# Performance work log

Measured on AMD Instinct MI355X. Metric: run time of the kernel, lower is better.

## Reference

```python
import jax, jax.numpy as jnp
import numpy as np

N = 50000      # nodes
E = 600000     # edges
F_ATOM = 78
D = 128        # hidden_dim = heads * head_dim
H = 8
C = D // H     # 16
ED = 12        # edge_dim
L = 4          # num_layers
B = 512        # graphs in batch
DFF = 4 * D
SCALE = 1.0 / float(np.sqrt(C))


def setup_inputs() -> dict:
    key = jax.random.key(0)
    ks = iter(jax.random.split(key, 128))
    rn = lambda s, sc=0.05: jax.random.normal(next(ks), s, jnp.float32) * sc
    inp = {
        "x": jax.random.normal(next(ks), (N, F_ATOM), jnp.float32),
        "edge_attr": jax.random.normal(next(ks), (E, ED), jnp.float32),
        "edge_index": jax.random.randint(next(ks), (2, E), 0, N),
        "batch": jnp.sort(jax.random.randint(next(ks), (N,), 0, B)),
        "Wemb": rn((F_ATOM, D)), "bemb": jnp.zeros((D,), jnp.float32),
        "Wout": rn((D, D)), "bout": jnp.zeros((D,), jnp.float32),
    }
    def stk(s, sc=0.05):
        return jnp.stack([rn(s, sc) for _ in range(L)])
    inp.update(
        Wq=stk((D, D)), bq=jnp.zeros((L, D), jnp.float32),
        Wk=stk((D, D)), bk=jnp.zeros((L, D), jnp.float32),
        Wv=stk((D, D)), bv=jnp.zeros((L, D), jnp.float32),
        We=stk((ED, D)), be=jnp.zeros((L, D), jnp.float32),
        Wskip=stk((D, D)), bskip=jnp.zeros((L, D), jnp.float32),
        Wbeta=stk((3 * D,)),
        g1=jnp.ones((L, D), jnp.float32), b1=jnp.zeros((L, D), jnp.float32),
        g2=jnp.ones((L, D), jnp.float32), b2=jnp.zeros((L, D), jnp.float32),
        Wf1=stk((D, DFF)), bf1=jnp.zeros((L, DFF), jnp.float32),
        Wf2=stk((DFF, D)), bf2=jnp.zeros((L, D), jnp.float32),
    )
    return inp


def _ln(x, g, b):
    mu = jnp.mean(x, -1, keepdims=True)
    var = jnp.mean((x - mu) ** 2, -1, keepdims=True)
    return (x - mu) * jax.lax.rsqrt(var + 1e-5) * g + b


def _seg_softmax(alpha, dst):
    # alpha: [E, H]; softmax over edges sharing a destination node
    m = jax.ops.segment_max(alpha, dst, num_segments=N)
    m = jnp.where(jnp.isfinite(m), m, 0.0)
    ex = jnp.exp(alpha - m[dst])
    den = jax.ops.segment_sum(ex, dst, num_segments=N)
    return ex / (den[dst] + 1e-16)


def _forward(x, edge_attr, Wemb, bemb, Wq, bq, Wk, bk, Wv, bv, We, be,
             Wskip, bskip, Wbeta, g1, b1, g2, b2, Wf1, bf1, Wf2, bf2,
             Wout, bout, edge_index, batch):
    src, dst = edge_index[0], edge_index[1]
    h = x @ Wemb + bemb                                    # [N, D]
    for l in range(L):
        q = (h @ Wq[l] + bq[l]).reshape(N, H, C)
        k = (h @ Wk[l] + bk[l]).reshape(N, H, C)
        v = (h @ Wv[l] + bv[l]).reshape(N, H, C)
        e = (edge_attr @ We[l] + be[l]).reshape(E, H, C)
        kj = k[src] + e                                    # [E, H, C]
        alpha = jnp.einsum('ehc,ehc->eh', q[dst], kj) * SCALE
        a = _seg_softmax(alpha, dst)                       # [E, H]
        msg = (v[src] + e) * a[:, :, None]                 # [E, H, C]
        agg = jax.ops.segment_sum(msg, dst, num_segments=N).reshape(N, D)
        xr = h @ Wskip[l] + bskip[l]                       # root/skip transform
        beta = jax.nn.sigmoid(
            jnp.concatenate([agg, xr, agg - xr], -1) @ Wbeta[l])[:, None]
        hc = beta * xr + (1.0 - beta) * agg                # beta gate
        h = _ln(hc + h, g1[l], b1[l])
        ff = jax.nn.relu(h @ Wf1[l] + bf1[l]) @ Wf2[l] + bf2[l]
        h = _ln(ff + h, g2[l], b2[l])
    cnt = jax.ops.segment_sum(jnp.ones((N,), h.dtype), batch, num_segments=B)
    pooled = jax.ops.segment_sum(h, batch, num_segments=B) / jnp.maximum(cnt, 1.0)[:, None]
    return pooled @ Wout + bout                            # [B, D]


def reference(x, edge_attr, edge_index, batch, Wemb, bemb, Wout, bout,
              Wq, bq, Wk, bk, Wv, bv, We, be, Wskip, bskip, Wbeta,
              g1, b1, g2, b2, Wf1, bf1, Wf2, bf2):
    return _forward(x, edge_attr, Wemb, bemb, Wq, bq, Wk, bk, Wv, bv, We, be,
                    Wskip, bskip, Wbeta, g1, b1, g2, b2, Wf1, bf1, Wf2, bf2,
                    Wout, bout, edge_index, batch)
```

## Files before the change

kernel.cpp:

```cpp
#include <hip/hip_runtime.h>
#include <math.h>

#define N_NODES 50000
#define N_EDGES 600000
#define FATOM   78
#define DIM     128
#define HEADS   8
#define EDIM    12
#define LAYERS  4
#define NBATCH  512
#define NDFF    512
#define ASCALE  0.25f

typedef __attribute__((ext_vector_type(8))) short bf16x8;
typedef __attribute__((ext_vector_type(4))) float f32x4;

__device__ __forceinline__ float sum16(float v){
  #pragma unroll
  for (int m=1;m<16;m<<=1) v += __shfl_xor(v, m);
  return v;
}
__device__ __forceinline__ short f2b(float f){
  unsigned int u = __builtin_bit_cast(unsigned int, f);
  u += 0x7fffu + ((u>>16)&1u);
  return (short)(u>>16);
}
__device__ __forceinline__ float b2f_lo(unsigned int u){ return __builtin_bit_cast(float, u<<16); }
__device__ __forceinline__ float b2f_hi(unsigned int u){ return __builtin_bit_cast(float, u & 0xffff0000u); }
__device__ __forceinline__ float b2f_s(short s){
  return __builtin_bit_cast(float, ((unsigned int)(unsigned short)s)<<16);
}
__device__ __forceinline__ void unp8(uint4 u, float* o){
  o[0]=b2f_lo(u.x); o[1]=b2f_hi(u.x); o[2]=b2f_lo(u.y); o[3]=b2f_hi(u.y);
  o[4]=b2f_lo(u.z); o[5]=b2f_hi(u.z); o[6]=b2f_lo(u.w); o[7]=b2f_hi(u.w);
}

__device__ __forceinline__ void gload16(const short* g, short* l){
  __builtin_amdgcn_global_load_lds(
      (const __attribute__((address_space(1))) void*)g,
      (__attribute__((address_space(3))) void*)l, 16, 0, 0);
}

__global__ void count_kernel(const int* __restrict__ ei, int* __restrict__ cnt){
  int e = blockIdx.x*256 + threadIdx.x;
  if (e < N_EDGES) atomicAdd(&cnt[ei[N_EDGES + e]], 1);
}

__global__ __launch_bounds__(1024) void scan1(const int* __restrict__ cnt,
                                              int* __restrict__ row_start, int* __restrict__ bsum){
  __shared__ int lds[1024];
  int gid = blockIdx.x*1024 + threadIdx.x;
  int v = (gid < N_NODES) ? cnt[gid] : 0;
  lds[threadIdx.x] = v; __syncthreads();
  for (int off=1; off<1024; off<<=1){
    int add = (threadIdx.x>=off)?lds[threadIdx.x-off]:0;
    __syncthreads();
    lds[threadIdx.x]+=add;
    __syncthreads();
  }
  if (gid < N_NODES) row_start[gid+1] = lds[threadIdx.x];
  if (threadIdx.x==1023) bsum[blockIdx.x] = lds[1023];
}
__global__ void scan2(int* __restrict__ bsum, int nb){
  int tid = threadIdx.x;
  int v = (tid < nb) ? bsum[tid] : 0;
  #pragma unroll
  for (int off=1; off<64; off<<=1){
    int u = __shfl_up(v, off);
    if (tid >= off) v += u;
  }
  if (tid < nb) bsum[tid] = v;
}
__global__ void scan3(int* __restrict__ row_start, const int* __restrict__ bsum){
  int gid = blockIdx.x*256 + threadIdx.x;
  if (gid == 0) row_start[0] = 0;
  if (gid < N_NODES){
    int blk = gid >> 10;
    if (blk > 0) row_start[gid+1] += bsum[blk-1];
  }
}

__global__ void scatter_kernel(const int* __restrict__ ei, const float* __restrict__ ea,
                               int* __restrict__ cnt2, const int* __restrict__ row_start,
                               int* __restrict__ src_s, short* __restrict__ ea_s){
  int e = blockIdx.x*256 + threadIdx.x;
  if (e < N_EDGES){
    int d = ei[N_EDGES + e];
    int pos = atomicAdd(&cnt2[d], 1);
    int p = row_start[d] + pos;
    src_s[p] = ei[e];
    const float* src = ea + (size_t)e*EDIM;
    unsigned int* dst = (unsigned int*)(ea_s + (size_t)p*EDIM);
    #pragma unroll
    for (int j=0;j<6;j++){
      unsigned int lo = (unsigned int)(unsigned short)f2b(src[2*j]);
      unsigned int hi = (unsigned int)(unsigned short)f2b(src[2*j+1]);
      dst[j] = lo | (hi<<16);
    }
  }
}

__global__ __launch_bounds__(256) void deg_hist(const int* __restrict__ cnt, int* __restrict__ dhist){
  __shared__ int lh[256];
  lh[threadIdx.x] = 0; __syncthreads();
  int n = blockIdx.x*256 + threadIdx.x;
  if (n < N_NODES){
    int d = cnt[n]; if (d > 255) d = 255;
    atomicAdd(&lh[d], 1);
  }
  __syncthreads();
  int c = lh[threadIdx.x];
  if (c) atomicAdd(&dhist[threadIdx.x], c);
}
__global__ __launch_bounds__(256) void deg_scan(const int* __restrict__ dhist, int* __restrict__ dstart){
  __shared__ int l[256];
  int t = threadIdx.x;
  int v = dhist[t];
  l[t] = v; __syncthreads();
  for (int off=1; off<256; off<<=1){
    int add = (t>=off)? l[t-off]:0;
    __syncthreads();
    l[t]+=add;
    __syncthreads();
  }
  dstart[t] = l[t]-v;
}
__global__ __launch_bounds__(256) void deg_place(const int* __restrict__ cnt, int* __restrict__ dcnt,
                                                 const int* __restrict__ dstart, int* __restrict__ perm){
  __shared__ int lh[256];
  __shared__ int lbase[256];
  __shared__ int lrank[256];
  int t = threadIdx.x;
  lh[t] = 0; lrank[t] = 0; __syncthreads();
  int n = blockIdx.x*256 + t;
  int d = -1;
  if (n < N_NODES){
    d = cnt[n]; if (d > 255) d = 255;
    atomicAdd(&lh[d], 1);
  }
  __syncthreads();
  int c = lh[t];
  lbase[t] = c ? atomicAdd(&dcnt[t], c) : 0;
  __syncthreads();
  if (n < N_NODES){
    int r = atomicAdd(&lrank[d], 1);
    perm[dstart[d] + lbase[d] + r] = n;
  }
}

__global__ __launch_bounds__(256) void pack_weights(
  const float* __restrict__ Wq, const float* __restrict__ Wk,
  const float* __restrict__ Wv, const float* __restrict__ Ws,
  const float* __restrict__ bq, const float* __restrict__ bk,
  const float* __restrict__ bv, const float* __restrict__ bs,
  const float* __restrict__ Wf1, const float* __restrict__ Wf2,
  short* __restrict__ wq_t, short* __restrict__ wf1_t, short* __restrict__ wf2_t,
  float* __restrict__ bqkvs)
{
  int l = blockIdx.y;
  int idx = blockIdx.x*256 + threadIdx.x;
  int sec = idx >> 16, r = idx & 65535;
  if (sec == 0){
    int n = r >> 7, k = r & 127;
    const float* W = (n<128)?Wq:(n<256)?Wk:(n<384)?Wv:Ws;
    float v = W[(size_t)l*16384 + k*128 + (n&127)];
    wq_t[(size_t)l*65536 + n*128 + k] = f2b(v);
    if (k == 0){
      const float* bb = (n<128)?bq:(n<256)?bk:(n<384)?bv:bs;
      bqkvs[l*512 + n] = bb[l*128 + (n&127)];
    }
  } else if (sec == 1){
    int n = r >> 7, k = r & 127;
    wf1_t[(size_t)l*65536 + n*128 + k] = f2b(Wf1[(size_t)l*65536 + k*512 + n]);
  } else {
    int n = r >> 9, k = r & 511;
    wf2_t[(size_t)l*65536 + n*512 + k] = f2b(Wf2[(size_t)l*65536 + k*128 + n]);
  }
}

__global__ void pack_emb(const float* __restrict__ Wemb, short* __restrict__ wemb_t){
  int idx = blockIdx.x*256 + threadIdx.x;
  int nn = idx >> 7, k = idx & 127;
  wemb_t[nn*128 + k] = (k < FATOM) ? f2b(Wemb[(size_t)k*DIM + nn]) : (short)0;
}

__global__ void cast_pad_x(const float* __restrict__ x, short* __restrict__ xb){
  int idx = blockIdx.x*256 + threadIdx.x;
  int n = idx >> 6, kp = (idx & 63)*2;
  if (n >= N_NODES) return;
  float v0 = (kp   < FATOM) ? x[(size_t)n*FATOM + kp]   : 0.f;
  float v1 = (kp+1 < FATOM) ? x[(size_t)n*FATOM + kp+1] : 0.f;
  unsigned int lo = (unsigned int)(unsigned short)f2b(v0);
  unsigned int hi = (unsigned int)(unsigned short)f2b(v1);
  *(unsigned int*)(xb + (size_t)n*128 + kp) = lo | (hi<<16);
}

__global__ __launch_bounds__(256) void gemm_k128(
    const short* __restrict__ A,
    const short* __restrict__ Bt,
    const float* __restrict__ bias,
    short* __restrict__ Cb,
    int Nrows, int M, int relu, int nbn)
{
  __shared__ short As[128*128];
  __shared__ short Bs[128*128];
  int tid  = threadIdx.x;
  int lane = tid & 63;
  int wave = tid >> 6;
  int wr = wave >> 1, wc = wave & 1;
  int bm = blockIdx.x * 128;
  int d  = lane & 15;
  int lr = lane >> 4;

  #pragma unroll
  for (int it=0; it<8; ++it){
    int r = wave*32 + it*4 + lr;
    int oct = (d & 8) | ((d & 7) ^ (r & 7));
    int gr = bm + r; if (gr >= Nrows) gr = Nrows-1;
    gload16(A + (size_t)gr*128 + oct*8, As + (wave*32 + it*4)*128);
  }

  for (int t=0; t<nbn; ++t){
    int bn = (blockIdx.y*nbn + t)*128;
    if (t) __syncthreads();
    #pragma unroll
    for (int it=0; it<8; ++it){
      int r = wave*32 + it*4 + lr;
      int oct = (d & 8) | ((d & 7) ^ (r & 7));
      gload16(Bt + (size_t)(bn + r)*128 + oct*8, Bs + (wave*32 + it*4)*128);
    }
    f32x4 zero = {0.f,0.f,0.f,0.f};
    f32x4 acc[4][4];
    #pragma unroll
    for (int m=0;m<4;m++)
      #pragma unroll
      for (int n=0;n<4;n++) acc[m][n] = zero;

    __syncthreads();

    #pragma unroll
    for (int ks=0; ks<4; ++ks){
      int oi = ks*4 + lr;
      bf16x8 af[4], bfv[4];
      #pragma unroll
      for (int m=0;m<4;m++){
        int row = wr*64 + m*16 + d;
        int slot = (oi&8) | ((oi&7) ^ (row&7));
        af[m] = *(const bf16x8*)(As + row*128 + slot*8);
      }
      #pragma unroll
      for (int n=0;n<4;n++){
        int col = wc*64 + n*16 + d;
        int slot = (oi&8) | ((oi&7) ^ (col&7));
        bfv[n] = *(const bf16x8*)(Bs + col*128 + slot*8);
      }
      #pragma unroll
      for (int m=0;m<4;m++)
        #pragma unroll
        for (int n=0;n<4;n++)
          acc[m][n] = __builtin_amdgcn_mfma_f32_16x16x32_bf16(af[m], bfv[n], acc[m][n], 0, 0, 0);
    }

    #pragma unroll
    for (int m=0;m<4;m++){
      #pragma unroll
      for (int n=0;n<4;n++){
        int col = bn + wc*64 + n*16 + d;
        float bval = bias[col];
        #pragma unroll
        for (int j=0;j<4;j++){
          int row = bm + wr*64 + m*16 + lr*4 + j;
          if (row < Nrows){
            float v = acc[m][n][j] + bval;
            if (relu) v = fmaxf(v, 0.f);
            Cb[(size_t)row*M + col] = f2b(v);
          }
        }
      }
    }
  }
}

__global__ __launch_bounds__(256) void gemm_ffn_ln(
    const short* __restrict__ W1t,
    const short* __restrict__ W2t,
    const float* __restrict__ bias1,
    const float* __restrict__ bias2,
    short* __restrict__ hb,
    const float* __restrict__ g, const float* __restrict__ b,
    int Nrows)
{
  __shared__ short As[64*128];
  __shared__ short Bs[128*128];
  __shared__ short F1[64*128];
  __shared__ float red[2][64][2];
  int tid  = threadIdx.x;
  int lane = tid & 63;
  int wave = tid >> 6;
  int wr = wave >> 1, wc = wave & 1;
  int bm = blockIdx.x * 64;
  int d  = lane & 15;
  int lr = lane >> 4;

  #pragma unroll
  for (int it=0; it<4; ++it){
    int rbase = wave*16 + it*4;
    int r = rbase + lr;
    int oct = (d & 8) | ((d & 7) ^ (r & 7));
    int gr = bm + r; if (gr >= Nrows) gr = Nrows-1;
    gload16(hb + (size_t)gr*128 + oct*8, As + rbase*128);
  }

  f32x4 zero = {0.f,0.f,0.f,0.f};
  f32x4 acc2[2][4];
  #pragma unroll
  for (int m=0;m<2;m++)
    #pragma unroll
    for (int n=0;n<4;n++) acc2[m][n] = zero;

  for (int t=0; t<4; ++t){
    #pragma unroll
    for (int it=0; it<8; ++it){
      int rbase = wave*32 + it*4;
      int r = rbase + lr;
      int oct = (d & 8) | ((d & 7) ^ (r & 7));
      gload16(W1t + (size_t)(t*128 + r)*128 + oct*8, Bs + rbase*128);
    }
    __syncthreads();

    f32x4 acc1[2][4];
    #pragma unroll
    for (int m=0;m<2;m++)
      #pragma unroll
      for (int n=0;n<4;n++) acc1[m][n] = zero;
    #pragma unroll
    for (int ks=0; ks<4; ++ks){
      int oi = ks*4 + lr;
      bf16x8 af[2], bfv[4];
      #pragma unroll
      for (int m=0;m<2;m++){
        int row = wr*32 + m*16 + d;
        int slot = (oi&8) | ((oi&7) ^ (row&7));
        af[m] = *(const bf16x8*)(As + row*128 + slot*8);
      }
      #pragma unroll
      for (int n=0;n<4;n++){
        int cn = wc*64 + n*16 + d;
        int slot = (oi&8) | ((oi&7) ^ (cn&7));
        bfv[n] = *(const bf16x8*)(Bs + cn*128 + slot*8);
      }
      #pragma unroll
      for (int m=0;m<2;m++)
        #pragma unroll
        for (int n=0;n<4;n++)
          acc1[m][n] = __builtin_amdgcn_mfma_f32_16x16x32_bf16(af[m], bfv[n], acc1[m][n], 0, 0, 0);
    }
    __syncthreads();

    #pragma unroll
    for (int m=0;m<2;m++){
      #pragma unroll
      for (int n=0;n<4;n++){
        int col = wc*64 + n*16 + d;
        float bv1 = bias1[t*128 + col];
        int oct2 = col >> 3, within = col & 7;
        #pragma unroll
        for (int j=0;j<4;j++){
          int row = wr*32 + m*16 + lr*4 + j;
          float v = fmaxf(acc1[m][n][j] + bv1, 0.f);
          int so = (oct2 & 8) | ((oct2 & 7) ^ (row & 7));
          F1[row*128 + so*8 + within] = f2b(v);
        }
      }
    }
    __syncthreads();

    #pragma unroll
    for (int ks=0; ks<4; ++ks){
      int oi = ks*4 + lr;
      bf16x8 af[2], bfv[4];
      #pragma unroll
      for (int m=0;m<2;m++){
        int row = wr*32 + m*16 + d;
        int slot = (oi&8) | ((oi&7) ^ (row&7));
        af[m] = *(const bf16x8*)(F1 + row*128 + slot*8);
      }
      #pragma unroll
      for (int n=0;n<4;n++){
        int col = wc*64 + n*16 + d;
        bfv[n] = *(const bf16x8*)(W2t + (size_t)col*512 + t*128 + oi*8);
      }
      #pragma unroll
      for (int m=0;m<2;m++)
        #pragma unroll
        for (int n=0;n<4;n++)
          acc2[m][n] = __builtin_amdgcn_mfma_f32_16x16x32_bf16(af[m], bfv[n], acc2[m][n], 0, 0, 0);
    }
  }

  #pragma unroll
  for (int m=0;m<2;m++){
    #pragma unroll
    for (int n=0;n<4;n++){
      int col = wc*64 + n*16 + d;
      float bval = bias2[col];
      #pragma unroll
      for (int j=0;j<4;j++){
        int row = wr*32 + m*16 + lr*4 + j;
        int grow = bm + row; if (grow >= Nrows) grow = Nrows-1;
        acc2[m][n][j] += bval + b2f_s(hb[(size_t)grow*DIM + col]);
      }
    }
  }
  #pragma unroll
  for (int m=0;m<2;m++){
    #pragma unroll
    for (int j=0;j<4;j++){
      float ps = 0.f, pq = 0.f;
      #pragma unroll
      for (int n=0;n<4;n++){ float v = acc2[m][n][j]; ps += v; pq += v*v; }
      #pragma unroll
      for (int msk=1; msk<16; msk<<=1){ ps += __shfl_xor(ps, msk); pq += __shfl_xor(pq, msk); }
      if (d == 0){
        int row = wr*32 + m*16 + lr*4 + j;
        red[wc][row][0] = ps;
        red[wc][row][1] = pq;
      }
    }
  }
  __syncthreads();
  #pragma unroll
  for (int m=0;m<2;m++){
    #pragma unroll
    for (int j=0;j<4;j++){
      int row = wr*32 + m*16 + lr*4 + j;
      float S = red[0][row][0] + red[1][row][0];
      float Q = red[0][row][1] + red[1][row][1];
      float mu  = S*(1.f/128.f);
      float var = fmaxf(Q*(1.f/128.f) - mu*mu, 0.f);
      float rr  = rsqrtf(var + 1e-5f);
      int grow = bm + row;
      if (grow < Nrows){
        #pragma unroll
        for (int n=0;n<4;n++){
          int col = wc*64 + n*16 + d;
          float o = (acc2[m][n][j]-mu)*rr*g[col] + b[col];
          hb[(size_t)grow*DIM + col] = f2b(o);
        }
      }
    }
  }
}

__global__ __launch_bounds__(256) void edge_attn_fused(
  const short* __restrict__ qkvx,
  const short* __restrict__ ea_s, const int* __restrict__ src_s,
  const float* __restrict__ Wel, const float* __restrict__ bel,
  const int* __restrict__ row_start, const int* __restrict__ perm,
  short* __restrict__ hb,
  const float* __restrict__ Wb, const float* __restrict__ g, const float* __restrict__ b)
{
  int wid = (blockIdx.x*256 + threadIdx.x) >> 4;
  if (wid >= N_NODES) return;
  int node = perm[N_NODES - 1 - wid];
  int ln = threadIdx.x & 15;
  int c0 = ln*8;

  const short* qrow = qkvx + (size_t)node*512;
  uint4 qu = *(const uint4*)(qrow + c0);
  float q0=b2f_lo(qu.x), q1=b2f_hi(qu.x), q2=b2f_lo(qu.y), q3=b2f_hi(qu.y);
  float q4=b2f_lo(qu.z), q5=b2f_hi(qu.z), q6=b2f_lo(qu.w), q7=b2f_hi(qu.w);

  float u[12];
  #pragma unroll
  for (int j=0;j<12;j++){
    float4 wA = *(const float4*)(Wel + j*DIM + c0);
    float4 wB = *(const float4*)(Wel + j*DIM + c0 + 4);
    float pp = q0*wA.x+q1*wA.y+q2*wA.z+q3*wA.w
             + q4*wB.x+q5*wB.y+q6*wB.z+q7*wB.w;
    u[j] = pp + __shfl_xor(pp,1);
  }
  float4 beA = *(const float4*)(bel + c0);
  float4 beB = *(const float4*)(bel + c0 + 4);
  float qbe;
  { float pp = q0*beA.x+q1*beA.y+q2*beA.z+q3*beA.w
             + q4*beB.x+q5*beB.y+q6*beB.z+q7*beB.w;
    qbe = pp + __shfl_xor(pp,1); }

  int rs = row_start[node], re = row_start[node+1];
  float den = 0.f;
  float av[8] = {0.f,0.f,0.f,0.f,0.f,0.f,0.f,0.f};
  float aEA[12] = {0.f,0.f,0.f,0.f,0.f,0.f,0.f,0.f,0.f,0.f,0.f,0.f};

  int i = rs;
  for (; i+2 <= re; i += 2){
    int s0 = src_s[i], s1 = src_s[i+1];
    const short* e0p = ea_s + (size_t)i*EDIM;
    uint2 a00 = *(const uint2*)(e0p);
    uint2 a01 = *(const uint2*)(e0p+4);
    uint2 a02 = *(const uint2*)(e0p+8);
    uint2 a10 = *(const uint2*)(e0p+12);
    uint2 a11 = *(const uint2*)(e0p+16);
    uint2 a12 = *(const uint2*)(e0p+20);
    const short* r0p = qkvx + (size_t)s0*512;
    const short* r1p = qkvx + (size_t)s1*512;
    uint4 ku0 = *(const uint4*)(r0p + 128 + c0);
    uint4 vu0 = *(const uint4*)(r0p + 256 + c0);
    uint4 ku1 = *(const uint4*)(r1p + 128 + c0);
    uint4 vu1 = *(const uint4*)(r1p + 256 + c0);

    float ea0[12], ea1[12];
    ea0[0]=b2f_lo(a00.x); ea0[1]=b2f_hi(a00.x); ea0[2]=b2f_lo(a00.y); ea0[3]=b2f_hi(a00.y);
    ea0[4]=b2f_lo(a01.x); ea0[5]=b2f_hi(a01.x); ea0[6]=b2f_lo(a01.y); ea0[7]=b2f_hi(a01.y);
    ea0[8]=b2f_lo(a02.x); ea0[9]=b2f_hi(a02.x); ea0[10]=b2f_lo(a02.y); ea0[11]=b2f_hi(a02.y);
    ea1[0]=b2f_lo(a10.x); ea1[1]=b2f_hi(a10.x); ea1[2]=b2f_lo(a10.y); ea1[3]=b2f_hi(a10.y);
    ea1[4]=b2f_lo(a11.x); ea1[5]=b2f_hi(a11.x); ea1[6]=b2f_lo(a11.y); ea1[7]=b2f_hi(a11.y);
    ea1[8]=b2f_lo(a12.x); ea1[9]=b2f_hi(a12.x); ea1[10]=b2f_lo(a12.y); ea1[11]=b2f_hi(a12.y);

    float pp0 = q0*b2f_lo(ku0.x) + q1*b2f_hi(ku0.x) + q2*b2f_lo(ku0.y) + q3*b2f_hi(ku0.y)
              + q4*b2f_lo(ku0.z) + q5*b2f_hi(ku0.z) + q6*b2f_lo(ku0.w) + q7*b2f_hi(ku0.w);
    float pp1 = q0*b2f_lo(ku1.x) + q1*b2f_hi(ku1.x) + q2*b2f_lo(ku1.y) + q3*b2f_hi(ku1.y)
              + q4*b2f_lo(ku1.z) + q5*b2f_hi(ku1.z) + q6*b2f_lo(ku1.w) + q7*b2f_hi(ku1.w);
    float al0 = pp0 + __shfl_xor(pp0,1) + qbe;
    float al1 = pp1 + __shfl_xor(pp1,1) + qbe;
    #pragma unroll
    for (int j=0;j<12;j++){ al0 += ea0[j]*u[j]; al1 += ea1[j]*u[j]; }
    float p0 = __expf(al0 * ASCALE);
    float p1 = __expf(al1 * ASCALE);
    den += p0 + p1;
    av[0] += p0*b2f_lo(vu0.x) + p1*b2f_lo(vu1.x);
    av[1] += p0*b2f_hi(vu0.x) + p1*b2f_hi(vu1.x);
    av[2] += p0*b2f_lo(vu0.y) + p1*b2f_lo(vu1.y);
    av[3] += p0*b2f_hi(vu0.y) + p1*b2f_hi(vu1.y);
    av[4] += p0*b2f_lo(vu0.z) + p1*b2f_lo(vu1.z);
    av[5] += p0*b2f_hi(vu0.z) + p1*b2f_hi(vu1.z);
    av[6] += p0*b2f_lo(vu0.w) + p1*b2f_lo(vu1.w);
    av[7] += p0*b2f_hi(vu0.w) + p1*b2f_hi(vu1.w);
    #pragma unroll
    for (int j=0;j<12;j++) aEA[j] += p0*ea0[j] + p1*ea1[j];
  }
  if (i < re){
    int s = src_s[i];
    const short* eap = ea_s + (size_t)i*EDIM;
    uint2 eu0 = *(const uint2*)(eap);
    uint2 eu1 = *(const uint2*)(eap+4);
    uint2 eu2 = *(const uint2*)(eap+8);
    float ea0[12];
    ea0[0]=b2f_lo(eu0.x); ea0[1]=b2f_hi(eu0.x); ea0[2]=b2f_lo(eu0.y); ea0[3]=b2f_hi(eu0.y);
    ea0[4]=b2f_lo(eu1.x); ea0[5]=b2f_hi(eu1.x); ea0[6]=b2f_lo(eu1.y); ea0[7]=b2f_hi(eu1.y);
    ea0[8]=b2f_lo(eu2.x); ea0[9]=b2f_hi(eu2.x); ea0[10]=b2f_lo(eu2.y); ea0[11]=b2f_hi(eu2.y);
    const short* srow = qkvx + (size_t)s*512;
    uint4 ku = *(const uint4*)(srow + 128 + c0);
    uint4 vu = *(const uint4*)(srow + 256 + c0);
    float pp = q0*b2f_lo(ku.x) + q1*b2f_hi(ku.x) + q2*b2f_lo(ku.y) + q3*b2f_hi(ku.y)
             + q4*b2f_lo(ku.z) + q5*b2f_hi(ku.z) + q6*b2f_lo(ku.w) + q7*b2f_hi(ku.w);
    float alpha = pp + __shfl_xor(pp,1) + qbe;
    #pragma unroll
    for (int j=0;j<12;j++) alpha += ea0[j]*u[j];
    float p = __expf(alpha * ASCALE);
    den += p;
    av[0] += p*b2f_lo(vu.x); av[1] += p*b2f_hi(vu.x);
    av[2] += p*b2f_lo(vu.y); av[3] += p*b2f_hi(vu.y);
    av[4] += p*b2f_lo(vu.z); av[5] += p*b2f_hi(vu.z);
    av[6] += p*b2f_lo(vu.w); av[7] += p*b2f_hi(vu.w);
    #pragma unroll
    for (int j=0;j<12;j++) aEA[j] += p*ea0[j];
  }

  float inv = 1.f/(den + 1e-16f);
  float gg[8];
  #pragma unroll
  for (int c=0;c<8;c++) gg[c] = av[c]*inv;
  #pragma unroll
  for (int j=0;j<12;j++){
    float wgt = aEA[j]*inv;
    float4 wA = *(const float4*)(Wel + j*DIM + c0);
    float4 wB = *(const float4*)(Wel + j*DIM + c0 + 4);
    gg[0]+=wgt*wA.x; gg[1]+=wgt*wA.y; gg[2]+=wgt*wA.z; gg[3]+=wgt*wA.w;
    gg[4]+=wgt*wB.x; gg[5]+=wgt*wB.y; gg[6]+=wgt*wB.z; gg[7]+=wgt*wB.w;
  }
  if (re > rs){
    gg[0]+=beA.x; gg[1]+=beA.y; gg[2]+=beA.z; gg[3]+=beA.w;
    gg[4]+=beB.x; gg[5]+=beB.y; gg[6]+=beB.z; gg[7]+=beB.w;
  }

  uint4 xu = *(const uint4*)(qrow + 384 + c0);
  float x[8];
  x[0]=b2f_lo(xu.x); x[1]=b2f_hi(xu.x); x[2]=b2f_lo(xu.y); x[3]=b2f_hi(xu.y);
  x[4]=b2f_lo(xu.z); x[5]=b2f_hi(xu.z); x[6]=b2f_lo(xu.w); x[7]=b2f_hi(xu.w);
  uint4 hu = *(const uint4*)(hb + (size_t)node*DIM + c0);
  float hv[8];
  unp8(hu, hv);
  float4 waA = *(const float4*)(Wb + c0),       waB = *(const float4*)(Wb + c0 + 4);
  float4 wxA = *(const float4*)(Wb + DIM + c0), wxB = *(const float4*)(Wb + DIM + c0 + 4);
  float4 wdA = *(const float4*)(Wb + 2*DIM + c0), wdB = *(const float4*)(Wb + 2*DIM + c0 + 4);
  float wa[8] = {waA.x,waA.y,waA.z,waA.w,waB.x,waB.y,waB.z,waB.w};
  float wx[8] = {wxA.x,wxA.y,wxA.z,wxA.w,wxB.x,wxB.y,wxB.z,wxB.w};
  float wd[8] = {wdA.x,wdA.y,wdA.z,wdA.w,wdB.x,wdB.y,wdB.z,wdB.w};
  float sacc = 0.f;
  #pragma unroll
  for (int c=0;c<8;c++) sacc += gg[c]*wa[c] + x[c]*wx[c] + (gg[c]-x[c])*wd[c];
  sacc = sum16(sacc);
  float beta = 1.f/(1.f + __expf(-sacc));
  float t[8], ts = 0.f;
  #pragma unroll
  for (int c=0;c<8;c++){ t[c] = beta*x[c] + (1.f-beta)*gg[c] + hv[c]; ts += t[c]; }
  float mu = sum16(ts)*(1.f/128.f);
  float vs = 0.f;
  #pragma unroll
  for (int c=0;c<8;c++){ t[c] -= mu; vs += t[c]*t[c]; }
  float var = sum16(vs)*(1.f/128.f);
  float r = rsqrtf(var + 1e-5f);
  float4 gA = *(const float4*)(g + c0), gB = *(const float4*)(g + c0 + 4);
  float4 bA = *(const float4*)(b + c0), bB = *(const float4*)(b + c0 + 4);
  float gv[8] = {gA.x,gA.y,gA.z,gA.w,gB.x,gB.y,gB.z,gB.w};
  float bv[8] = {bA.x,bA.y,bA.z,bA.w,bB.x,bB.y,bB.z,bB.w};
  float o[8];
  #pragma unroll
  for (int c=0;c<8;c++) o[c] = t[c]*r*gv[c] + bv[c];
  uint4 ou;
  ou.x = (unsigned int)(unsigned short)f2b(o[0]) | ((unsigned int)(unsigned short)f2b(o[1])<<16);
  ou.y = (unsigned int)(unsigned short)f2b(o[2]) | ((unsigned int)(unsigned short)f2b(o[3])<<16);
  ou.z = (unsigned int)(unsigned short)f2b(o[4]) | ((unsigned int)(unsigned short)f2b(o[5])<<16);
  ou.w = (unsigned int)(unsigned short)f2b(o[6]) | ((unsigned int)(unsigned short)f2b(o[7])<<16);
  *(uint4*)(hb + (size_t)node*DIM + c0) = ou;
}

__global__ __launch_bounds__(128) void pool_out(
  const short* __restrict__ hb, const int* __restrict__ batch,
  const float* __restrict__ Wout, const float* __restrict__ bout,
  float* __restrict__ out)
{
  int bidx = blockIdx.x;
  int d = threadIdx.x;
  __shared__ int seg[2];
  __shared__ float p[DIM];
  if (d < 2){
    int target = bidx + d;
    int lo = 0, hi = N_NODES;
    while (lo < hi){ int mid = (lo+hi)>>1; if (batch[mid] < target) lo = mid+1; else hi = mid; }
    seg[d] = lo;
  }
  __syncthreads();
  int lo = seg[0], hi = seg[1];
  float s = 0.f;
  for (int n=lo; n<hi; ++n) s += b2f_s(hb[(size_t)n*DIM + d]);
  float cnt = (float)(hi - lo);
  p[d] = s / fmaxf(cnt, 1.f);
  __syncthreads();
  float o = bout[d];
  #pragma unroll 8
  for (int kk=0; kk<DIM; ++kk) o += p[kk]*Wout[kk*DIM + d];
  out[bidx*DIM + d] = o;
}

extern "C" void kernel_launch(void* const* d_in, const int* in_sizes, int n_in,
                              void* d_out, int out_size, void* d_ws, size_t ws_size,
                              hipStream_t stream)
{
  const float* x     = (const float*)d_in[0];
  const float* ea    = (const float*)d_in[1];
  const int*   ei    = (const int*)d_in[2];
  const int*   batch = (const int*)d_in[3];
  const float* Wemb  = (const float*)d_in[4];
  const float* bemb  = (const float*)d_in[5];
  const float* Wout  = (const float*)d_in[6];
  const float* bout  = (const float*)d_in[7];
  const float* Wq    = (const float*)d_in[8];
  const float* bq    = (const float*)d_in[9];
  const float* Wk    = (const float*)d_in[10];
  const float* bk    = (const float*)d_in[11];
  const float* Wv    = (const float*)d_in[12];
  const float* bv    = (const float*)d_in[13];
  const float* We    = (const float*)d_in[14];
  const float* be    = (const float*)d_in[15];
  const float* Wskip = (const float*)d_in[16];
  const float* bskip = (const float*)d_in[17];
  const float* Wbeta = (const float*)d_in[18];
  const float* g1    = (const float*)d_in[19];
  const float* b1    = (const float*)d_in[20];
  const float* g2    = (const float*)d_in[21];
  const float* b2    = (const float*)d_in[22];
  const float* Wf1   = (const float*)d_in[23];
  const float* bf1   = (const float*)d_in[24];
  const float* Wf2   = (const float*)d_in[25];
  const float* bf2   = (const float*)d_in[26];
  float* out = (float*)d_out;

  float* ws     = (float*)d_ws;
  float* bqkvs  = ws;
  short* ea_s   = (short*)(bqkvs + LAYERS*512);
  short* hb     = ea_s + (size_t)N_EDGES*EDIM;
  short* region = hb + (size_t)N_NODES*DIM;
  short* xb     = region + (size_t)N_NODES*NDFF;
  short* wemb_t = xb + (size_t)N_NODES*DIM;
  short* wq_t   = wemb_t + DIM*DIM;
  short* wf1_t  = wq_t  + (size_t)LAYERS*NDFF*DIM;
  short* wf2_t  = wf1_t + (size_t)LAYERS*NDFF*DIM;
  int*   cnt       = (int*)(wf2_t + (size_t)LAYERS*NDFF*DIM);
  int*   cnt2      = cnt + N_NODES;
  int*   row_start = cnt2 + N_NODES;
  int*   bsum      = row_start + N_NODES + 1;
  int*   dhist     = bsum + 64;
  int*   dcnt      = dhist + 256;
  int*   dstart    = dcnt + 256;
  int*   node_perm = dstart + 256;
  int*   src_s     = node_perm + N_NODES;

  hipMemsetAsync(cnt,  0, N_NODES*sizeof(int), stream);
  hipMemsetAsync(cnt2, 0, N_NODES*sizeof(int), stream);
  hipMemsetAsync(dhist, 0, 512*sizeof(int), stream);

  const int NB_SCAN = (N_NODES + 1023)/1024;
  const int NB_DEG  = (N_NODES + 255)/256;
  count_kernel<<<(N_EDGES+255)/256, 256, 0, stream>>>(ei, cnt);
  scan1<<<NB_SCAN, 1024, 0, stream>>>(cnt, row_start, bsum);
  scan2<<<1, 64, 0, stream>>>(bsum, NB_SCAN);
  scan3<<<(N_NODES+255)/256, 256, 0, stream>>>(row_start, bsum);
  deg_hist<<<NB_DEG, 256, 0, stream>>>(cnt, dhist);
  deg_scan<<<1, 256, 0, stream>>>(dhist, dstart);
  deg_place<<<NB_DEG, 256, 0, stream>>>(cnt, dcnt, dstart, node_perm);
  scatter_kernel<<<(N_EDGES+255)/256, 256, 0, stream>>>(ei, ea, cnt2, row_start, src_s, ea_s);

  pack_weights<<<dim3(768, LAYERS), 256, 0, stream>>>(
      Wq, Wk, Wv, Wskip, bq, bk, bv, bskip, Wf1, Wf2, wq_t, wf1_t, wf2_t, bqkvs);
  pack_emb<<<64, 256, 0, stream>>>(Wemb, wemb_t);
  cast_pad_x<<<(N_NODES*64 + 255)/256, 256, 0, stream>>>(x, xb);

  int gM  = (N_NODES + 127)/128;
  int gM64 = (N_NODES + 63)/64;
  int attnBlocks = (N_NODES*16 + 255)/256;

  gemm_k128<<<dim3(gM, 1), 256, 0, stream>>>(xb, wemb_t, bemb, hb, N_NODES, DIM, 0, 1);

  for (int l=0; l<LAYERS; ++l){
    gemm_k128<<<dim3(gM, 2), 256, 0, stream>>>(
        hb, wq_t + (size_t)l*NDFF*DIM, bqkvs + l*512, region,
        N_NODES, NDFF, 0, 2);

    edge_attn_fused<<<attnBlocks, 256, 0, stream>>>(
        region, ea_s, src_s, We + (size_t)l*EDIM*DIM, be + l*DIM, row_start, node_perm,
        hb, Wbeta + l*3*DIM, g1 + l*DIM, b1 + l*DIM);

    gemm_ffn_ln<<<dim3(gM64, 1), 256, 0, stream>>>(
        wf1_t + (size_t)l*NDFF*DIM, wf2_t + (size_t)l*DIM*NDFF,
        bf1 + l*NDFF, bf2 + l*DIM, hb,
        g2 + l*DIM, b2 + l*DIM, N_NODES);
  }

  pool_out<<<NBATCH, 128, 0, stream>>>(hb, batch, Wout, bout, out);
}
```

Baseline: 783.9 us.

## Split QKV projection output into separate K/V and Q/skip buffers for gather locality

A new QKV GEMM writes K and V into one 256-wide buffer and Q and skip into another, replacing a single 512-wide row. The point is that the edge-attention gather of K and V from source nodes touches a compact 512-byte row, which should improve cache and TLB locality. The edge loop also prefetches the next pair of source indices, and pool_out now uses 256 threads split into two halves. The costs are a second output buffer and a branchy epilogue in the GEMM that picks the destination per column block.

```diff
diff --git a/kernel.cpp b/kernel.cpp
--- a/kernel.cpp
+++ b/kernel.cpp
@@ -281,6 +281,96 @@
   }
 }
 
+__global__ __launch_bounds__(256) void gemm_qkvs(
+    const short* __restrict__ A,
+    const short* __restrict__ Bt,
+    const float* __restrict__ bias,
+    short* __restrict__ kv, short* __restrict__ qx,
+    int Nrows, int nbn)
+{
+  __shared__ short As[128*128];
+  __shared__ short Bs[128*128];
+  int tid  = threadIdx.x;
+  int lane = tid & 63;
+  int wave = tid >> 6;
+  int wr = wave >> 1, wc = wave & 1;
+  int bm = blockIdx.x * 128;
+  int d  = lane & 15;
+  int lr = lane >> 4;
+
+  #pragma unroll
+  for (int it=0; it<8; ++it){
+    int r = wave*32 + it*4 + lr;
+    int oct = (d & 8) | ((d & 7) ^ (r & 7));
+    int gr = bm + r; if (gr >= Nrows) gr = Nrows-1;
+    gload16(A + (size_t)gr*128 + oct*8, As + (wave*32 + it*4)*128);
+  }
+
+  for (int t=0; t<nbn; ++t){
+    int bn = (blockIdx.y*nbn + t)*128;
+    if (t) __syncthreads();
+    #pragma unroll
+    for (int it=0; it<8; ++it){
+      int r = wave*32 + it*4 + lr;
+      int oct = (d & 8) | ((d & 7) ^ (r & 7));
+      gload16(Bt + (size_t)(bn + r)*128 + oct*8, Bs + (wave*32 + it*4)*128);
+    }
+    f32x4 zero = {0.f,0.f,0.f,0.f};
+    f32x4 acc[4][4];
+    #pragma unroll
+    for (int m=0;m<4;m++)
+      #pragma unroll
+      for (int n=0;n<4;n++) acc[m][n] = zero;
+
+    __syncthreads();
+
+    #pragma unroll
+    for (int ks=0; ks<4; ++ks){
+      int oi = ks*4 + lr;
+      bf16x8 af[4], bfv[4];
+      #pragma unroll
+      for (int m=0;m<4;m++){
+        int row = wr*64 + m*16 + d;
+        int slot = (oi&8) | ((oi&7) ^ (row&7));
+        af[m] = *(const bf16x8*)(As + row*128 + slot*8);
+      }
+      #pragma unroll
+      for (int n=0;n<4;n++){
+        int col = wc*64 + n*16 + d;
+        int slot = (oi&8) | ((oi&7) ^ (col&7));
+        bfv[n] = *(const bf16x8*)(Bs + col*128 + slot*8);
+      }
+      #pragma unroll
+      for (int m=0;m<4;m++)
+        #pragma unroll
+        for (int n=0;n<4;n++)
+          acc[m][n] = __builtin_amdgcn_mfma_f32_16x16x32_bf16(af[m], bfv[n], acc[m][n], 0, 0, 0);
+    }
+
+    short* dst; int coff;
+    if (bn == 0)       { dst = qx; coff = 0;    }
+    else if (bn < 384) { dst = kv; coff = -128; }
+    else               { dst = qx; coff = -256; }
+
+    #pragma unroll
+    for (int m=0;m<4;m++){
+      #pragma unroll
+      for (int n=0;n<4;n++){
+        int col = bn + wc*64 + n*16 + d;
+        float bval = bias[col];
+        #pragma unroll
+        for (int j=0;j<4;j++){
+          int row = bm + wr*64 + m*16 + lr*4 + j;
+          if (row < Nrows){
+            float v = acc[m][n][j] + bval;
+            dst[(size_t)row*256 + col + coff] = f2b(v);
+          }
+        }
+      }
+    }
+  }
+}
+
 __global__ __launch_bounds__(256) void gemm_ffn_ln(
     const short* __restrict__ W1t,
     const short* __restrict__ W2t,
@@ -453,7 +543,8 @@
 }
 
 __global__ __launch_bounds__(256) void edge_attn_fused(
-  const short* __restrict__ qkvx,
+  const short* __restrict__ kv,
+  const short* __restrict__ qx,
   const short* __restrict__ ea_s, const int* __restrict__ src_s,
   const float* __restrict__ Wel, const float* __restrict__ bel,
   const int* __restrict__ row_start, const int* __restrict__ perm,
@@ -466,7 +557,7 @@
   int ln = threadIdx.x & 15;
   int c0 = ln*8;
 
-  const short* qrow = qkvx + (size_t)node*512;
+  const short* qrow = qx + (size_t)node*256;
   uint4 qu = *(const uint4*)(qrow + c0);
   float q0=b2f_lo(qu.x), q1=b2f_hi(qu.x), q2=b2f_lo(qu.y), q3=b2f_hi(qu.y);
   float q4=b2f_lo(qu.z), q5=b2f_hi(qu.z), q6=b2f_lo(qu.w), q7=b2f_hi(qu.w);
@@ -492,9 +583,13 @@
   float av[8] = {0.f,0.f,0.f,0.f,0.f,0.f,0.f,0.f};
   float aEA[12] = {0.f,0.f,0.f,0.f,0.f,0.f,0.f,0.f,0.f,0.f,0.f,0.f};
 
-  int i = rs;
-  for (; i+2 <= re; i += 2){
-    int s0 = src_s[i], s1 = src_s[i+1];
+  int npairs = (re - rs) >> 1;
+  int s0 = 0, s1 = 0;
+  if (npairs > 0){ s0 = src_s[rs]; s1 = src_s[rs+1]; }
+  for (int p=0; p<npairs; ++p){
+    int i = rs + p*2;
+    int s0n = 0, s1n = 0;
+    if (p+1 < npairs){ s0n = src_s[i+2]; s1n = src_s[i+3]; }
     const short* e0p = ea_s + (size_t)i*EDIM;
     uint2 a00 = *(const uint2*)(e0p);
     uint2 a01 = *(const uint2*)(e0p+4);
@@ -502,12 +597,12 @@
     uint2 a10 = *(const uint2*)(e0p+12);
     uint2 a11 = *(const uint2*)(e0p+16);
     uint2 a12 = *(const uint2*)(e0p+20);
-    const short* r0p = qkvx + (size_t)s0*512;
-    const short* r1p = qkvx + (size_t)s1*512;
-    uint4 ku0 = *(const uint4*)(r0p + 128 + c0);
-    uint4 vu0 = *(const uint4*)(r0p + 256 + c0);
-    uint4 ku1 = *(const uint4*)(r1p + 128 + c0);
-    uint4 vu1 = *(const uint4*)(r1p + 256 + c0);
+    const short* r0p = kv + (size_t)s0*256;
+    const short* r1p = kv + (size_t)s1*256;
+    uint4 ku0 = *(const uint4*)(r0p + c0);
+    uint4 vu0 = *(const uint4*)(r0p + 128 + c0);
+    uint4 ku1 = *(const uint4*)(r1p + c0);
+    uint4 vu1 = *(const uint4*)(r1p + 128 + c0);
 
     float ea0[12], ea1[12];
     ea0[0]=b2f_lo(a00.x); ea0[1]=b2f_hi(a00.x); ea0[2]=b2f_lo(a00.y); ea0[3]=b2f_hi(a00.y);
@@ -538,33 +633,37 @@
     av[7] += p0*b2f_hi(vu0.w) + p1*b2f_hi(vu1.w);
     #pragma unroll
     for (int j=0;j<12;j++) aEA[j] += p0*ea0[j] + p1*ea1[j];
-  }
-  if (i < re){
-    int s = src_s[i];
-    const short* eap = ea_s + (size_t)i*EDIM;
-    uint2 eu0 = *(const uint2*)(eap);
-    uint2 eu1 = *(const uint2*)(eap+4);
-    uint2 eu2 = *(const uint2*)(eap+8);
-    float ea0[12];
-    ea0[0]=b2f_lo(eu0.x); ea0[1]=b2f_hi(eu0.x); ea0[2]=b2f_lo(eu0.y); ea0[3]=b2f_hi(eu0.y);
-    ea0[4]=b2f_lo(eu1.x); ea0[5]=b2f_hi(eu1.x); ea0[6]=b2f_lo(eu1.y); ea0[7]=b2f_hi(eu1.y);
-    ea0[8]=b2f_lo(eu2.x); ea0[9]=b2f_hi(eu2.x); ea0[10]=b2f_lo(eu2.y); ea0[11]=b2f_hi(eu2.y);
-    const short* srow = qkvx + (size_t)s*512;
-    uint4 ku = *(const uint4*)(srow + 128 + c0);
-    uint4 vu = *(const uint4*)(srow + 256 + c0);
-    float pp = q0*b2f_lo(ku.x) + q1*b2f_hi(ku.x) + q2*b2f_lo(ku.y) + q3*b2f_hi(ku.y)
-             + q4*b2f_lo(ku.z) + q5*b2f_hi(ku.z) + q6*b2f_lo(ku.w) + q7*b2f_hi(ku.w);
-    float alpha = pp + __shfl_xor(pp,1) + qbe;
-    #pragma unroll
-    for (int j=0;j<12;j++) alpha += ea0[j]*u[j];
-    float p = __expf(alpha * ASCALE);
-    den += p;
-    av[0] += p*b2f_lo(vu.x); av[1] += p*b2f_hi(vu.x);
-    av[2] += p*b2f_lo(vu.y); av[3] += p*b2f_hi(vu.y);
-    av[4] += p*b2f_lo(vu.z); av[5] += p*b2f_hi(vu.z);
-    av[6] += p*b2f_lo(vu.w); av[7] += p*b2f_hi(vu.w);
-    #pragma unroll
-    for (int j=0;j<12;j++) aEA[j] += p*ea0[j];
+    s0 = s0n; s1 = s1n;
+  }
+  {
+    int i = rs + npairs*2;
+    if (i < re){
+      int s = src_s[i];
+      const short* eap = ea_s + (size_t)i*EDIM;
+      uint2 eu0 = *(const uint2*)(eap);
+      uint2 eu1 = *(const uint2*)(eap+4);
+      uint2 eu2 = *(const uint2*)(eap+8);
+      float ea0[12];
+      ea0[0]=b2f_lo(eu0.x); ea0[1]=b2f_hi(eu0.x); ea0[2]=b2f_lo(eu0.y); ea0[3]=b2f_hi(eu0.y);
+      ea0[4]=b2f_lo(eu1.x); ea0[5]=b2f_hi(eu1.x); ea0[6]=b2f_lo(eu1.y); ea0[7]=b2f_hi(eu1.y);
+      ea0[8]=b2f_lo(eu2.x); ea0[9]=b2f_hi(eu2.x); ea0[10]=b2f_lo(eu2.y); ea0[11]=b2f_hi(eu2.y);
+      const short* srow = kv + (size_t)s*256;
+      uint4 ku = *(const uint4*)(srow + c0);
+      uint4 vu = *(const uint4*)(srow + 128 + c0);
+      float pp = q0*b2f_lo(ku.x) + q1*b2f_hi(ku.x) + q2*b2f_lo(ku.y) + q3*b2f_hi(ku.y)
+               + q4*b2f_lo(ku.z) + q5*b2f_hi(ku.z) + q6*b2f_lo(ku.w) + q7*b2f_hi(ku.w);
+      float alpha = pp + __shfl_xor(pp,1) + qbe;
+      #pragma unroll
+      for (int j=0;j<12;j++) alpha += ea0[j]*u[j];
+      float p = __expf(alpha * ASCALE);
+      den += p;
+      av[0] += p*b2f_lo(vu.x); av[1] += p*b2f_hi(vu.x);
+      av[2] += p*b2f_lo(vu.y); av[3] += p*b2f_hi(vu.y);
+      av[4] += p*b2f_lo(vu.z); av[5] += p*b2f_hi(vu.z);
+      av[6] += p*b2f_lo(vu.w); av[7] += p*b2f_hi(vu.w);
+      #pragma unroll
+      for (int j=0;j<12;j++) aEA[j] += p*ea0[j];
+    }
   }
 
   float inv = 1.f/(den + 1e-16f);
@@ -584,7 +683,7 @@
     gg[4]+=beB.x; gg[5]+=beB.y; gg[6]+=beB.z; gg[7]+=beB.w;
   }
 
-  uint4 xu = *(const uint4*)(qrow + 384 + c0);
+  uint4 xu = *(const uint4*)(qrow + 128 + c0);
   float x[8];
   x[0]=b2f_lo(xu.x); x[1]=b2f_hi(xu.x); x[2]=b2f_lo(xu.y); x[3]=b2f_hi(xu.y);
   x[4]=b2f_lo(xu.z); x[5]=b2f_hi(xu.z); x[6]=b2f_lo(xu.w); x[7]=b2f_hi(xu.w);
@@ -626,32 +725,40 @@
   *(uint4*)(hb + (size_t)node*DIM + c0) = ou;
 }
 
-__global__ __launch_bounds__(128) void pool_out(
+__global__ __launch_bounds__(256) void pool_out(
   const short* __restrict__ hb, const int* __restrict__ batch,
   const float* __restrict__ Wout, const float* __restrict__ bout,
   float* __restrict__ out)
 {
   int bidx = blockIdx.x;
-  int d = threadIdx.x;
+  int d = threadIdx.x & 127;
+  int half = threadIdx.x >> 7;
   __shared__ int seg[2];
+  __shared__ float psum[2][DIM];
   __shared__ float p[DIM];
-  if (d < 2){
-    int target = bidx + d;
+  if (threadIdx.x < 2){
+    int target = bidx + threadIdx.x;
     int lo = 0, hi = N_NODES;
     while (lo < hi){ int mid = (lo+hi)>>1; if (batch[mid] < target) lo = mid+1; else hi = mid; }
-    seg[d] = lo;
+    seg[threadIdx.x] = lo;
   }
   __syncthreads();
   int lo = seg[0], hi = seg[1];
   float s = 0.f;
-  for (int n=lo; n<hi; ++n) s += b2f_s(hb[(size_t)n*DIM + d]);
-  float cnt = (float)(hi - lo);
-  p[d] = s / fmaxf(cnt, 1.f);
+  for (int n=lo+half; n<hi; n+=2) s += b2f_s(hb[(size_t)n*DIM + d]);
+  psum[half][d] = s;
   __syncthreads();
-  float o = bout[d];
+  if (half == 0){
+    float cnt = (float)(hi - lo);
+    p[d] = (psum[0][d] + psum[1][d]) / fmaxf(cnt, 1.f);
+  }
+  __syncthreads();
+  float o = 0.f;
   #pragma unroll 8
-  for (int kk=0; kk<DIM; ++kk) o += p[kk]*Wout[kk*DIM + d];
-  out[bidx*DIM + d] = o;
+  for (int kk=half*64; kk<half*64+64; ++kk) o += p[kk]*Wout[kk*DIM + d];
+  psum[half][d] = o;
+  __syncthreads();
+  if (half == 0) out[bidx*DIM + d] = psum[0][d] + psum[1][d] + bout[d];
 }
 
 extern "C" void kernel_launch(void* const* d_in, const int* in_sizes, int n_in,
@@ -691,8 +798,9 @@
   float* bqkvs  = ws;
   short* ea_s   = (short*)(bqkvs + LAYERS*512);
   short* hb     = ea_s + (size_t)N_EDGES*EDIM;
-  short* region = hb + (size_t)N_NODES*DIM;
-  short* xb     = region + (size_t)N_NODES*NDFF;
+  short* kv     = hb + (size_t)N_NODES*DIM;
+  short* qx     = kv + (size_t)N_NODES*256;
+  short* xb     = qx + (size_t)N_NODES*256;
   short* wemb_t = xb + (size_t)N_NODES*DIM;
   short* wq_t   = wemb_t + DIM*DIM;
   short* wf1_t  = wq_t  + (size_t)LAYERS*NDFF*DIM;
@@ -734,12 +842,11 @@
   gemm_k128<<<dim3(gM, 1), 256, 0, stream>>>(xb, wemb_t, bemb, hb, N_NODES, DIM, 0, 1);
 
   for (int l=0; l<LAYERS; ++l){
-    gemm_k128<<<dim3(gM, 2), 256, 0, stream>>>(
-        hb, wq_t + (size_t)l*NDFF*DIM, bqkvs + l*512, region,
-        N_NODES, NDFF, 0, 2);
+    gemm_qkvs<<<dim3(gM, 2), 256, 0, stream>>>(
+        hb, wq_t + (size_t)l*NDFF*DIM, bqkvs + l*512, kv, qx, N_NODES, 2);
 
     edge_attn_fused<<<attnBlocks, 256, 0, stream>>>(
-        region, ea_s, src_s, We + (size_t)l*EDIM*DIM, be + l*DIM, row_start, node_perm,
+        kv, qx, ea_s, src_s, We + (size_t)l*EDIM*DIM, be + l*DIM, row_start, node_perm,
         hb, Wbeta + l*3*DIM, g1 + l*DIM, b1 + l*DIM);
 
     gemm_ffn_ln<<<dim3(gM64, 1), 256, 0, stream>>>(
@@ -748,5 +855,5 @@
         g2 + l*DIM, b2 + l*DIM, N_NODES);
   }
 
-  pool_out<<<NBATCH, 128, 0, stream>>>(hb, batch, Wout, bout, out);
-}
+  pool_out<<<NBATCH, 256, 0, stream>>>(hb, batch, Wout, bout, out);
+}
```

New measurement: 751.3 us (median of 3 runs). 1.04x faster.
